# Kernel tuning notes

Measured on AMD Instinct MI355X. Metric: run time of the kernel, lower is better.

## Reference

```python
import jax, jax.numpy as jnp
import numpy as np

B, H, W, C_IN, C_HID = 32, 64, 64, 384, 128

def setup_inputs() -> dict:
    key = jax.random.key(0)
    k0, k1, k2 = jax.random.split(key, 3)
    dino_features = jax.random.normal(k0, (B, H, W, C_IN), dtype=jnp.float32)
    # Xavier-uniform(gain=0.5) bounds for conv weights, HWIO layout
    fan1 = C_IN * 9 + C_HID * 9
    lim1 = 0.5 * np.sqrt(6.0 / fan1)
    W1 = jax.random.uniform(k1, (3, 3, C_IN, C_HID), minval=-lim1, maxval=lim1, dtype=jnp.float32)
    b1 = jnp.zeros((C_HID,), dtype=jnp.float32)
    fan2 = C_HID + 1
    lim2 = 0.5 * np.sqrt(6.0 / fan2)
    W2 = jax.random.uniform(k2, (1, 1, C_HID, 1), minval=-lim2, maxval=lim2, dtype=jnp.float32)
    b2 = jnp.zeros((1,), dtype=jnp.float32)
    return {"dino_features": dino_features, "W1": W1, "b1": b1, "W2": W2, "b2": b2}

def _conv(x, w, pad):
    # x: NHWC, w: HWIO -> NHWC
    return jax.lax.conv_general_dilated(
        x, w, window_strides=(1, 1), padding=pad,
        dimension_numbers=("NHWC", "HWIO", "NHWC"))

def reference(dino_features, W1, b1, W2, b2):
    # conv3x3 (pad 1) -> ReLU -> conv1x1 -> sigmoid; output (B,H,W,1)
    h = jax.nn.relu(_conv(dino_features, W1, ((1, 1), (1, 1))) + b1)
    logits = _conv(h, W2, ((0, 0), (0, 0))) + b2
    return jax.nn.sigmoid(logits)
```

## Files before the change

kernel.cpp:

```cpp
#include <hip/hip_runtime.h>
#include <hip/hip_bf16.h>
#include <math.h>


typedef __attribute__((ext_vector_type(8))) unsigned short ushort8;
typedef __attribute__((ext_vector_type(8))) __bf16 bf16x8;
typedef __attribute__((ext_vector_type(4))) float floatx4;

#define HPX 324
#define BUFE 10368

static __device__ __forceinline__ unsigned short f2bf_rne(float f) {
  union { float f; unsigned int u; } x; x.f = f;
  unsigned int u = x.u;
  return (unsigned short)((u + 0x7fffu + ((u >> 16) & 1u)) >> 16);
}

static __device__ __forceinline__ ushort8 pack8(const float* v) {
  ushort8 r;
#pragma unroll
  for (int i = 0; i < 4; ++i) {
    __hip_bfloat162 p = __float22bfloat162_rn(make_float2(v[2 * i], v[2 * i + 1]));
    union { __hip_bfloat162 b; unsigned int u; } c;
    c.b = p;
    r[2 * i] = (unsigned short)(c.u & 0xffffu);
    r[2 * i + 1] = (unsigned short)(c.u >> 16);
  }
  return r;
}

__global__ void prep_w1_kernel(const float* __restrict__ W1,
                               unsigned short* __restrict__ W1b) {
  __shared__ unsigned short tile[32 * 128];
  const int kk = blockIdx.x;
  const int o = kk / 12;
  const int chunk = kk - o * 12;
  const float* src = W1 + (o * 384 + chunk * 32) * 128;
  const int t = threadIdx.x;
#pragma unroll
  for (int i = 0; i < 16; ++i) {
    int idx = t + i * 256;
    int c = idx >> 7;
    int n = idx & 127;
    tile[n * 32 + c] = f2bf_rne(src[idx]);
  }
  __syncthreads();
  unsigned short* dst = W1b + kk * 4096;
#pragma unroll
  for (int i = 0; i < 16; ++i) {
    int idx = t + i * 256;
    dst[idx] = tile[idx];
  }
}

__global__ __launch_bounds__(512, 4) void conv_fused_kernel(
    const float* __restrict__ x, const unsigned short* __restrict__ W1b,
    const float* __restrict__ b1, const float* __restrict__ W2,
    const float* __restrict__ b2, float* __restrict__ out) {
  __shared__ alignas(16) unsigned short Ah[2 * BUFE];
  __shared__ float hsum[256 * 8];

  const int t = threadIdx.x;
  const int w = t >> 6;
  const int lane = t & 63;
  const int g = lane >> 4;
  const int lr = lane & 15;

  const int img = blockIdx.x >> 4;
  const int tileId = blockIdx.x & 15;
  const int ty0 = (tileId >> 2) << 4;
  const int tx0 = (tileId & 3) << 4;

  int smask = 0;
  int soff[3];
#pragma unroll
  for (int j = 0; j < 3; ++j) {
    int item = t + (j << 9);
    int px = item >> 2, sub = item & 3;
    int hy = (px * 57) >> 10;
    int hx = px - hy * 18;
    int iy = ty0 + hy - 1, ix = tx0 + hx - 1;
    int v = (item < 1296) && ((unsigned)iy < 64u) && ((unsigned)ix < 64u);
    smask |= (v << j);
    int iyc = v ? iy : 0, ixc = v ? ix : 0;
    soff[j] = ((((img << 6) + iyc) << 6) + ixc) * 384 + sub * 8;
  }

  const int boff = ((w * 16 + lr) << 5) + (g << 3);
  const int aoffl = (lr << 5) + (g << 3);

  floatx4 acc[16] = {};

  const float b1v = b1[w * 16 + lr];
  const float w2v = W2[w * 16 + lr];

  float sg1[8];
  float sr[2][8];

  {
    if (smask & 1) {
      *(float4*)&sg1[0] = *(const float4*)(x + soff[0]);
      *(float4*)&sg1[4] = *(const float4*)(x + soff[0] + 4);
    } else {
#pragma unroll
      for (int e = 0; e < 8; ++e) sg1[e] = 0.0f;
    }
#pragma unroll
    for (int j = 0; j < 2; ++j) {
      const int jj = 1 + j;
      if ((smask >> jj) & 1) {
        *(float4*)&sr[j][0] = *(const float4*)(x + soff[jj]);
        *(float4*)&sr[j][4] = *(const float4*)(x + soff[jj] + 4);
      } else {
#pragma unroll
        for (int e = 0; e < 8; ++e) sr[j][e] = 0.0f;
      }
    }
    *(ushort8*)&Ah[t << 3] = pack8(sg1);
    *(ushort8*)&Ah[(t + 512) << 3] = pack8(sr[0]);
    if (t < 272) *(ushort8*)&Ah[(t + 1024) << 3] = pack8(sr[1]);
  }
  __syncthreads();

  for (int c = 0; c < 12; ++c) {
    const int rb = (c & 1) * BUFE;
    const int wb = BUFE - rb;
    const int choff = (c + 1) << 5;
    const bool pf = (c < 11);

#pragma unroll
    for (int ox = 0; ox < 3; ++ox) {
      bf16x8 bf[3];
#pragma unroll
      for (int oy = 0; oy < 3; ++oy) {
        const unsigned short* bp =
            W1b + (((oy * 3 + ox) * 12 + c) << 12) + boff;
        bf[oy] = *(const bf16x8*)bp;
      }

      if (ox == 0) {
        if (pf) {
          if (smask & 1) {
            *(float4*)&sg1[0] = *(const float4*)(x + soff[0] + choff);
            *(float4*)&sg1[4] = *(const float4*)(x + soff[0] + choff + 4);
          } else {
#pragma unroll
            for (int e = 0; e < 8; ++e) sg1[e] = 0.0f;
          }
        }
      } else if (ox == 1) {
        if (pf) {
          *(ushort8*)&Ah[wb + (t << 3)] = pack8(sg1);
#pragma unroll
          for (int j = 0; j < 2; ++j) {
            const int jj = 1 + j;
            if ((smask >> jj) & 1) {
              *(float4*)&sr[j][0] = *(const float4*)(x + soff[jj] + choff);
              *(float4*)&sr[j][4] = *(const float4*)(x + soff[jj] + choff + 4);
            } else {
#pragma unroll
              for (int e = 0; e < 8; ++e) sr[j][e] = 0.0f;
            }
          }
        }
      } else {
        if (pf) {
          *(ushort8*)&Ah[wb + ((t + 512) << 3)] = pack8(sr[0]);
          if (t < 272) *(ushort8*)&Ah[wb + ((t + 1024) << 3)] = pack8(sr[1]);
        }
      }

      __builtin_amdgcn_s_setprio(1);
#pragma unroll
      for (int h = 0; h < 18; ++h) {
        const bf16x8 af =
            *(const bf16x8*)&Ah[rb + ((h * 18 + ox) << 5) + aoffl];
#pragma unroll
        for (int oy = 0; oy < 3; ++oy) {
          const int mi = h - oy;
          if (mi >= 0 && mi < 16) {
            acc[mi] = __builtin_amdgcn_mfma_f32_16x16x32_bf16(
                af, bf[oy], acc[mi], 0, 0, 0);
          }
        }
      }
      __builtin_amdgcn_s_setprio(0);
    }
    __syncthreads();
  }

#pragma unroll
  for (int mi = 0; mi < 16; ++mi) {
#pragma unroll
    for (int r = 0; r < 4; ++r) {
      float h0 = fmaxf(acc[mi][r] + b1v, 0.0f);
      float v = h0 * w2v;
      v += __shfl_xor(v, 1);
      v += __shfl_xor(v, 2);
      v += __shfl_xor(v, 4);
      v += __shfl_xor(v, 8);
      if (lr == 0) {
        int m = mi * 16 + g * 4 + r;
        hsum[m * 8 + w] = v;
      }
    }
  }
  __syncthreads();
  if (t < 256) {
    float4 p0 = *(const float4*)&hsum[t * 8];
    float4 p1 = *(const float4*)&hsum[t * 8 + 4];
    float s = p0.x + p0.y + p0.z + p0.w + p1.x + p1.y + p1.z + p1.w + b2[0];
    float sig = 1.0f / (1.0f + expf(-s));
    int prow = t >> 4, pcol = t & 15;
    out[((((img << 6) + ty0 + prow) << 6) + tx0 + pcol)] = sig;
  }
}

extern "C" void kernel_launch(void* const* d_in, const int* in_sizes, int n_in,
                              void* d_out, int out_size, void* d_ws, size_t ws_size,
                              hipStream_t stream) {
  const float* x  = (const float*)d_in[0];
  const float* W1 = (const float*)d_in[1];
  const float* b1 = (const float*)d_in[2];
  const float* W2 = (const float*)d_in[3];
  const float* b2 = (const float*)d_in[4];
  float* out = (float*)d_out;
  unsigned short* W1b = (unsigned short*)d_ws;

  prep_w1_kernel<<<108, 256, 0, stream>>>(W1, W1b);
  conv_fused_kernel<<<512, 512, 0, stream>>>(x, W1b, b1, W2, b2, out);
}
```

Measured before the change: 320.4 us.

## Split waves into 2x4 grid over rows and output channels for operand reuse

Each wave used to own 16 output channels across all 16 tile rows. It now owns 32 channels across 8 rows, with waves arranged 2 (rows) by 4 (channels). Each A fragment now feeds two MFMAs, and each wave reads 10 A rows instead of 18 per ox step, which cuts redundant LDS reads and halo overhead. In exchange it loads twice the B fragments per wave, and the launch-bounds occupancy hint drops from 4 to 3, which allows more registers per thread. The final reduction across waves shrinks from 8 partials to 4.

```diff
diff --git a/kernel.cpp b/kernel.cpp
--- a/kernel.cpp
+++ b/kernel.cpp
@@ -53,15 +53,17 @@
   }
 }
 
-__global__ __launch_bounds__(512, 4) void conv_fused_kernel(
+__global__ __launch_bounds__(512, 3) void conv_fused_kernel(
     const float* __restrict__ x, const unsigned short* __restrict__ W1b,
     const float* __restrict__ b1, const float* __restrict__ W2,
     const float* __restrict__ b2, float* __restrict__ out) {
   __shared__ alignas(16) unsigned short Ah[2 * BUFE];
-  __shared__ float hsum[256 * 8];
+  __shared__ float hsum[256 * 4];
 
   const int t = threadIdx.x;
   const int w = t >> 6;
+  const int wm = w >> 2;
+  const int wn = w & 3;
   const int lane = t & 63;
   const int g = lane >> 4;
   const int lr = lane & 15;
@@ -86,13 +88,15 @@
     soff[j] = ((((img << 6) + iyc) << 6) + ixc) * 384 + sub * 8;
   }
 
-  const int boff = ((w * 16 + lr) << 5) + (g << 3);
+  const int boff = ((wn * 32 + lr) << 5) + (g << 3);
   const int aoffl = (lr << 5) + (g << 3);
 
-  floatx4 acc[16] = {};
-
-  const float b1v = b1[w * 16 + lr];
-  const float w2v = W2[w * 16 + lr];
+  floatx4 acc[8][2] = {};
+
+  const float b1v0 = b1[wn * 32 + lr];
+  const float b1v1 = b1[wn * 32 + 16 + lr];
+  const float w2v0 = W2[wn * 32 + lr];
+  const float w2v1 = W2[wn * 32 + 16 + lr];
 
   float sg1[8];
   float sr[2][8];
@@ -130,12 +134,13 @@
 
 #pragma unroll
     for (int ox = 0; ox < 3; ++ox) {
-      bf16x8 bf[3];
+      bf16x8 bf[3][2];
 #pragma unroll
       for (int oy = 0; oy < 3; ++oy) {
         const unsigned short* bp =
             W1b + (((oy * 3 + ox) * 12 + c) << 12) + boff;
-        bf[oy] = *(const bf16x8*)bp;
+        bf[oy][0] = *(const bf16x8*)bp;
+        bf[oy][1] = *(const bf16x8*)(bp + 512);
       }
 
       if (ox == 0) {
@@ -172,15 +177,18 @@
 
       __builtin_amdgcn_s_setprio(1);
 #pragma unroll
-      for (int h = 0; h < 18; ++h) {
+      for (int hl = 0; hl < 10; ++hl) {
+        const int hg = wm * 8 + hl;
         const bf16x8 af =
-            *(const bf16x8*)&Ah[rb + ((h * 18 + ox) << 5) + aoffl];
+            *(const bf16x8*)&Ah[rb + ((hg * 18 + ox) << 5) + aoffl];
 #pragma unroll
         for (int oy = 0; oy < 3; ++oy) {
-          const int mi = h - oy;
-          if (mi >= 0 && mi < 16) {
-            acc[mi] = __builtin_amdgcn_mfma_f32_16x16x32_bf16(
-                af, bf[oy], acc[mi], 0, 0, 0);
+          const int mi = hl - oy;
+          if (mi >= 0 && mi < 8) {
+            acc[mi][0] = __builtin_amdgcn_mfma_f32_16x16x32_bf16(
+                af, bf[oy][0], acc[mi][0], 0, 0, 0);
+            acc[mi][1] = __builtin_amdgcn_mfma_f32_16x16x32_bf16(
+                af, bf[oy][1], acc[mi][1], 0, 0, 0);
           }
         }
       }
@@ -190,26 +198,26 @@
   }
 
 #pragma unroll
-  for (int mi = 0; mi < 16; ++mi) {
+  for (int mi = 0; mi < 8; ++mi) {
 #pragma unroll
     for (int r = 0; r < 4; ++r) {
-      float h0 = fmaxf(acc[mi][r] + b1v, 0.0f);
-      float v = h0 * w2v;
+      float h0 = fmaxf(acc[mi][0][r] + b1v0, 0.0f);
+      float h1 = fmaxf(acc[mi][1][r] + b1v1, 0.0f);
+      float v = h0 * w2v0 + h1 * w2v1;
       v += __shfl_xor(v, 1);
       v += __shfl_xor(v, 2);
       v += __shfl_xor(v, 4);
       v += __shfl_xor(v, 8);
       if (lr == 0) {
-        int m = mi * 16 + g * 4 + r;
-        hsum[m * 8 + w] = v;
+        int m = (wm * 8 + mi) * 16 + g * 4 + r;
+        hsum[m * 4 + wn] = v;
       }
     }
   }
   __syncthreads();
   if (t < 256) {
-    float4 p0 = *(const float4*)&hsum[t * 8];
-    float4 p1 = *(const float4*)&hsum[t * 8 + 4];
-    float s = p0.x + p0.y + p0.z + p0.w + p1.x + p1.y + p1.z + p1.w + b2[0];
+    float4 p = *(const float4*)&hsum[t * 4];
+    float s = p.x + p.y + p.z + p.w + b2[0];
     float sig = 1.0f / (1.0f + expf(-s));
     int prow = t >> 4, pcol = t & 15;
     out[((((img << 6) + ty0 + prow) << 6) + tx0 + pcol)] = sig;
```

After: 342.4 us. +6.9%, slower.
